# Kernel optimization log

Hardware: AMD Instinct MI355X
Metric: run time of the kernel (lower is better)

Reference implementation:

```python
import jax, jax.numpy as jnp
import numpy as np

NDIM = 3        # coordinate dimensionality
KS = 3          # kernel size per dim (odd)
DIL = 0.05      # dilation (spacing between kernel cells)
MAXD = 1.0      # max_distance cap on SDF values
G = 64          # SDF grid resolution per dim
NSDF = 8        # number of SDF grids
OUT = 32        # out_channels
K = KS ** NDIM  # 27 kernel cells
CELL = 0.031    # grid cell size -> grid extent ~2.0


def _kernel_offsets():
    r = (jnp.arange(KS, dtype=jnp.float32) - KS // 2) * DIL
    ox, oy, oz = jnp.meshgrid(r, r, r, indexing='ij')
    return jnp.stack([ox.ravel(), oy.ravel(), oz.ravel()], -1)  # [K,3]


def _rot_inv(q, v):
    # rotate v by the inverse of quaternion q (xyzw layout), broadcasting
    u = -q[..., :3]
    w = q[..., 3:4]
    c = jnp.cross(u, v)
    return v + 2.0 * jnp.cross(u, c + w * v)


def setup_inputs() -> dict:
    key = jax.random.key(0)
    ks = jax.random.split(key, 8)
    B, N, M = 2, 50000, 4
    extent = G * CELL  # ~2.0, local grid extent
    locs = jax.random.uniform(ks[0], (B, N, NDIM), jnp.float32) * extent
    idxs = jax.random.randint(ks[1], (B, M), 0, NSDF).astype(jnp.int32)
    trans = jax.random.uniform(ks[2], (B, M, NDIM), jnp.float32) * 0.2
    quat = jax.random.normal(ks[3], (B, M, 4), jnp.float32)
    quat = quat / jnp.linalg.norm(quat, axis=-1, keepdims=True)
    poses = jnp.concatenate([trans, quat], axis=-1)  # [B,M,7] = trans + quat(xyzw)
    scales = jax.random.uniform(ks[4], (B, M), jnp.float32) + 0.5
    sdf_grid = jax.random.normal(ks[5], (NSDF, G, G, G), jnp.float32) * 0.3 + 0.2
    cell_sizes = jnp.full((NSDF,), CELL, jnp.float32)
    weight = jax.random.normal(ks[6], (OUT, K), jnp.float32) * 0.1
    bias = jax.random.normal(ks[7], (OUT,), jnp.float32) * 0.1
    return dict(locs=locs, idxs=idxs, poses=poses, scales=scales,
                sdf_grid=sdf_grid, cell_sizes=cell_sizes, weight=weight, bias=bias)


def _convsdf(locs, idxs, poses, scales, sdf_grid, cell_sizes, weight, bias):
    offs = _kernel_offsets()                                  # [K,3]
    p = locs[:, :, None, :] + offs[None, None, :, :]          # [B,N,K,3] kernel-cell points
    t = poses[:, :, :NDIM]                                    # [B,M,3]
    q = poses[:, :, NDIM:]                                    # [B,M,4]
    # transform each kernel-cell point into each SDF's local frame
    r = p[:, :, :, None, :] - t[:, None, None, :, :]          # [B,N,K,M,3]
    r = _rot_inv(q[:, None, None, :, :], r)
    sc = scales[:, None, None, :, None]                       # [B,1,1,M,1]
    r = r / sc
    cs = cell_sizes[idxs][:, None, None, :, None]             # [B,1,1,M,1]
    gc = r / cs - 0.5                                         # grid coords (values at cell centers)
    inb = jnp.all((r >= 0.0) & (r <= G * cs), axis=-1)        # [B,N,K,M] inside grid?
    gcc = jnp.clip(gc, 0.0, G - 1.0)
    i0 = jnp.clip(jnp.floor(gcc), 0.0, G - 2.0).astype(jnp.int32)
    fr = gcc - i0.astype(jnp.float32)
    flat = sdf_grid.reshape(-1)
    jb = idxs.astype(jnp.int32)[:, None, None, :]             # [B,1,1,M]
    val = jnp.zeros(inb.shape, jnp.float32)
    # trilinear interpolation: 8 corner gathers
    for dx in (0, 1):
        wx = fr[..., 0] if dx else 1.0 - fr[..., 0]
        for dy in (0, 1):
            wy = fr[..., 1] if dy else 1.0 - fr[..., 1]
            for dz in (0, 1):
                wz = fr[..., 2] if dz else 1.0 - fr[..., 2]
                fi = ((jb * G + i0[..., 0] + dx) * G + i0[..., 1] + dy) * G + i0[..., 2] + dz
                val = val + wx * wy * wz * jnp.take(flat, fi)
    # scaled SDF value; out-of-grid -> max_distance, then min over objects, cap
    val = jnp.where(inb, val * sc[..., 0], MAXD)
    d = jnp.minimum(jnp.min(val, axis=-1), MAXD)              # [B,N,K]
    return jnp.einsum('bnk,ok->bno', d, weight) + bias        # [B,N,OUT]


def reference(locs, idxs, poses, scales, sdf_grid, cell_sizes, weight, bias):
    return _convsdf(locs, idxs, poses, scales, sdf_grid, cell_sizes, weight, bias)
```

## Files before the change

### kernel.cpp

```cpp
#include <hip/hip_runtime.h>
#include <math.h>

#define KK 27
#define MM 4
#define OUTC 32
#define GG 64
#define DILF 0.05f
#define MAXDF 1.0f
#define MU 4e-3f

static __device__ inline bool exact_inb(float lx, float ly, float lz,
                                        float ox, float oy, float oz,
                                        float tx, float ty, float tz,
                                        float qx, float qy, float qz, float qw,
                                        float sc, float gcs) {
#pragma clang fp contract(off)
    float px = lx + ox, py = ly + oy, pz = lz + oz;
    float vx = px - tx, vy = py - ty, vz = pz - tz;
    float ux = -qx, uy = -qy, uz = -qz;
    float cx = uy * vz - uz * vy;
    float cy = uz * vx - ux * vz;
    float cz = ux * vy - uy * vx;
    float twx = cx + qw * vx;
    float twy = cy + qw * vy;
    float twz = cz + qw * vz;
    float rx = vx + 2.0f * (uy * twz - uz * twy);
    float ry = vy + 2.0f * (uz * twx - ux * twz);
    float rz = vz + 2.0f * (ux * twy - uy * twx);
    rx = rx / sc; ry = ry / sc; rz = rz / sc;
    return (rx >= 0.0f) & (rx <= gcs) & (ry >= 0.0f) & (ry <= gcs) &
           (rz >= 0.0f) & (rz <= gcs);
}

__global__ __launch_bounds__(256) void convsdf_kernel(
    const float* __restrict__ locs, const int* __restrict__ idxs,
    const float* __restrict__ poses, const float* __restrict__ scales,
    const float* __restrict__ sdf, const float* __restrict__ cells,
    const float* __restrict__ weight, const float* __restrict__ bias,
    float* __restrict__ out, int N) {
    __shared__ float4 s_ro[MM][KK];
    __shared__ float4 s_off[KK];
    __shared__ float4 s_wT4[KK * OUTC / 4];
    __shared__ float  s_bias[OUTC];
    __shared__ float  s_t[MM][3];
    __shared__ float  s_q[MM][4];
    __shared__ float  s_sc[MM];
    __shared__ float  s_gcs[MM];
    __shared__ float  s_invscs[MM];
    __shared__ int    s_goff[MM];

    const int b = blockIdx.y;
    const int tid = threadIdx.x;

    float* s_wT = (float*)s_wT4;
    for (int i = tid; i < KK * OUTC; i += 256) {
        int k = i >> 5, o = i & 31;
        s_wT[i] = weight[o * KK + k];
    }
    if (tid < OUTC) s_bias[tid] = bias[tid];
    if (tid < KK) {
        int kx = tid / 9, ky = (tid / 3) % 3, kz = tid % 3;
        s_off[tid] = make_float4((float)(kx - 1) * DILF, (float)(ky - 1) * DILF,
                                 (float)(kz - 1) * DILF, 0.0f);
    }
    if (tid >= 128 && tid < 128 + MM) {
        int m = tid - 128;
        const float* pp = poses + (b * MM + m) * 7;
        float sc = scales[b * MM + m];
        int gi = idxs[b * MM + m];
        float cs = cells[gi];
        s_t[m][0] = pp[0]; s_t[m][1] = pp[1]; s_t[m][2] = pp[2];
        s_q[m][0] = pp[3]; s_q[m][1] = pp[4]; s_q[m][2] = pp[5]; s_q[m][3] = pp[6];
        s_sc[m] = sc;
        s_gcs[m] = (float)GG * cs;
        s_invscs[m] = 1.0f / (sc * cs);
        s_goff[m] = gi * GG * GG * GG;
    }
    __syncthreads();

    if (tid < MM * KK) {
        int m = tid / KK, k = tid - m * KK;
        float4 off = s_off[k];
        float qx = s_q[m][0], qy = s_q[m][1], qz = s_q[m][2], qw = s_q[m][3];
        float ux = -qx, uy = -qy, uz = -qz;
        float vx = off.x, vy = off.y, vz = off.z;
        float cx = uy * vz - uz * vy + qw * vx;
        float cy = uz * vx - ux * vz + qw * vy;
        float cz = ux * vy - uy * vx + qw * vz;
        float rx = vx + 2.0f * (uy * cz - uz * cy);
        float ry = vy + 2.0f * (uz * cx - ux * cz);
        float rz = vz + 2.0f * (ux * cy - uy * cx);
        float f = s_invscs[m];
        s_ro[m][k] = make_float4(rx * f, ry * f, rz * f, 0.0f);
    }
    __syncthreads();

    const int pl = tid >> 2;
    const int m  = tid & 3;
    const int n  = blockIdx.x * 64 + pl;
    if (n >= N) return;

    const float* lp = locs + (size_t)(b * N + n) * 3;
    float lx = lp[0], ly = lp[1], lz = lp[2];

    float tx = s_t[m][0], ty = s_t[m][1], tz = s_t[m][2];
    float qx = s_q[m][0], qy = s_q[m][1], qz = s_q[m][2], qw = s_q[m][3];
    float sc = s_sc[m], gcs = s_gcs[m];
    float bux, buy, buz;
    {
        float vx = lx - tx, vy = ly - ty, vz = lz - tz;
        float ux = -qx, uy = -qy, uz = -qz;
        float cx = uy * vz - uz * vy + qw * vx;
        float cy = uz * vx - ux * vz + qw * vy;
        float cz = ux * vy - uy * vx + qw * vz;
        float rx = vx + 2.0f * (uy * cz - uz * cy);
        float ry = vy + 2.0f * (uz * cx - ux * cz);
        float rz = vz + 2.0f * (ux * cy - uy * cx);
        float f = s_invscs[m];
        bux = rx * f; buy = ry * f; buz = rz * f;
    }
    const float* gbase = sdf + s_goff[m];

    float acc[8];
#pragma unroll
    for (int j = 0; j < 8; ++j) acc[j] = s_bias[m * 8 + j];

#pragma unroll 3
    for (int k = 0; k < KK; ++k) {
        float4 ro = s_ro[m][k];
        float ux = bux + ro.x;
        float uy = buy + ro.y;
        float uz = buz + ro.z;
        float mn = fminf(fminf(ux, uy), uz);
        float mx = fmaxf(fmaxf(ux, uy), uz);
        bool inb = (mn >= 0.0f) & (mx <= 64.0f);
        float a0 = fminf(fminf(fabsf(ux), fabsf(uy)), fabsf(uz));
        float a1 = fminf(fminf(fabsf(ux - 64.0f), fabsf(uy - 64.0f)),
                         fabsf(uz - 64.0f));
        if (fminf(a0, a1) < MU) {
            float4 ofk = s_off[k];
            inb = exact_inb(lx, ly, lz, ofk.x, ofk.y, ofk.z,
                            tx, ty, tz, qx, qy, qz, qw, sc, gcs);
        }
        float v = MAXDF;
        if (inb) {
            float gx = fminf(fmaxf(ux - 0.5f, 0.0f), 63.0f);
            float gy = fminf(fmaxf(uy - 0.5f, 0.0f), 63.0f);
            float gz = fminf(fmaxf(uz - 0.5f, 0.0f), 63.0f);
            int ix = min((int)gx, 62);
            int iy = min((int)gy, 62);
            int iz = min((int)gz, 62);
            float fx = gx - (float)ix;
            float fy = gy - (float)iy;
            float fz = gz - (float)iz;
            const float* g = gbase + ((ix * GG + iy) * GG + iz);
            float v000 = g[0], v001 = g[1];
            float v010 = g[GG], v011 = g[GG + 1];
            float v100 = g[GG * GG], v101 = g[GG * GG + 1];
            float v110 = g[GG * GG + GG], v111 = g[GG * GG + GG + 1];
            float c00 = v000 + fz * (v001 - v000);
            float c01 = v010 + fz * (v011 - v010);
            float c10 = v100 + fz * (v101 - v100);
            float c11 = v110 + fz * (v111 - v110);
            float c0 = c00 + fy * (c01 - c00);
            float c1 = c10 + fy * (c11 - c10);
            v = (c0 + fx * (c1 - c0)) * sc;
        }
        float dk = v;
        dk = fminf(dk, __shfl_xor(dk, 1, 4));
        dk = fminf(dk, __shfl_xor(dk, 2, 4));
        float4 w0 = s_wT4[k * (OUTC / 4) + m * 2 + 0];
        float4 w1 = s_wT4[k * (OUTC / 4) + m * 2 + 1];
        acc[0] += dk * w0.x; acc[1] += dk * w0.y;
        acc[2] += dk * w0.z; acc[3] += dk * w0.w;
        acc[4] += dk * w1.x; acc[5] += dk * w1.y;
        acc[6] += dk * w1.z; acc[7] += dk * w1.w;
    }

    float* op = out + (size_t)(b * N + n) * OUTC + m * 8;
    *(float4*)&op[0] = make_float4(acc[0], acc[1], acc[2], acc[3]);
    *(float4*)&op[4] = make_float4(acc[4], acc[5], acc[6], acc[7]);
}

extern "C" void kernel_launch(void* const* d_in, const int* in_sizes, int n_in,
                              void* d_out, int out_size, void* d_ws, size_t ws_size,
                              hipStream_t stream) {
    const float* locs   = (const float*)d_in[0];
    const int*   idxs   = (const int*)d_in[1];
    const float* poses  = (const float*)d_in[2];
    const float* scales = (const float*)d_in[3];
    const float* sdf    = (const float*)d_in[4];
    const float* cells  = (const float*)d_in[5];
    const float* weight = (const float*)d_in[6];
    const float* bias   = (const float*)d_in[7];
    float* out = (float*)d_out;

    int B = in_sizes[1] / MM;
    int N = in_sizes[0] / (3 * B);

    dim3 grid((N + 63) / 64, B);
    convsdf_kernel<<<grid, 256, 0, stream>>>(locs, idxs, poses, scales, sdf,
                                             cells, weight, bias, out, N);
}
```

Measured before the change: 28.68 us.

## Repack SDF grids into fp16 corner-octet layout for single-load trilinear gathers

Adds a per-call repack kernel that stores all eight trilinear corner values of each voxel as packed fp16 in one 16-byte record, restricted to grids referenced by idxs. The main kernel then fetches one uint4 per sample instead of eight scattered floats. This is meant to cut gather latency and transaction count, at the cost of an extra kernel launch, tens of MB of workspace writes each call, and fp16 rounding of SDF values. It falls back to the direct kernel when the workspace is too small.

Result: slower. 35.58 us (+24.1%).

```diff
diff --git a/kernel.cpp b/kernel.cpp
--- a/kernel.cpp
+++ b/kernel.cpp
@@ -1,10 +1,12 @@
 #include <hip/hip_runtime.h>
+#include <hip/hip_fp16.h>
 #include <math.h>
 
 #define KK 27
 #define MM 4
 #define OUTC 32
 #define GG 64
+#define GG3 (GG * GG * GG)
 #define DILF 0.05f
 #define MAXDF 1.0f
 #define MU 4e-3f
@@ -32,7 +34,194 @@
            (rz >= 0.0f) & (rz <= gcs);
 }
 
-__global__ __launch_bounds__(256) void convsdf_kernel(
+__global__ __launch_bounds__(256) void repack_kernel(
+    const float* __restrict__ sdf, const int* __restrict__ idxs,
+    uint4* __restrict__ oct, int nslots) {
+    const int j = blockIdx.y;
+    __shared__ int ref;
+    if (threadIdx.x == 0) {
+        int r = 0;
+        for (int s = 0; s < nslots; ++s) r |= (idxs[s] == j) ? 1 : 0;
+        ref = r;
+    }
+    __syncthreads();
+    if (!ref) return;
+
+    int i = blockIdx.x * 256 + threadIdx.x;
+    int x = i >> 12, y = (i >> 6) & 63, z = i & 63;
+    int xp = min(x + 1, 63), yp = min(y + 1, 63), zp = min(z + 1, 63);
+    const float* g = sdf + (size_t)j * GG3;
+    float v000 = g[(x * GG + y) * GG + z];
+    float v001 = g[(x * GG + y) * GG + zp];
+    float v010 = g[(x * GG + yp) * GG + z];
+    float v011 = g[(x * GG + yp) * GG + zp];
+    float v100 = g[(xp * GG + y) * GG + z];
+    float v101 = g[(xp * GG + y) * GG + zp];
+    float v110 = g[(xp * GG + yp) * GG + z];
+    float v111 = g[(xp * GG + yp) * GG + zp];
+    __half2 h0 = __floats2half2_rn(v000, v001);
+    __half2 h1 = __floats2half2_rn(v010, v011);
+    __half2 h2 = __floats2half2_rn(v100, v101);
+    __half2 h3 = __floats2half2_rn(v110, v111);
+    uint4 o;
+    o.x = *(unsigned int*)&h0;
+    o.y = *(unsigned int*)&h1;
+    o.z = *(unsigned int*)&h2;
+    o.w = *(unsigned int*)&h3;
+    oct[(size_t)j * GG3 + i] = o;
+}
+
+__global__ __launch_bounds__(256) void convsdf_oct_kernel(
+    const float* __restrict__ locs, const int* __restrict__ idxs,
+    const float* __restrict__ poses, const float* __restrict__ scales,
+    const uint4* __restrict__ oct, const float* __restrict__ cells,
+    const float* __restrict__ weight, const float* __restrict__ bias,
+    float* __restrict__ out, int N) {
+    __shared__ float4 s_ro[MM][KK];
+    __shared__ float4 s_off[KK];
+    __shared__ float4 s_wT4[KK * OUTC / 4];
+    __shared__ float  s_bias[OUTC];
+    __shared__ float  s_t[MM][3];
+    __shared__ float  s_q[MM][4];
+    __shared__ float  s_sc[MM];
+    __shared__ float  s_gcs[MM];
+    __shared__ float  s_invscs[MM];
+    __shared__ int    s_goff[MM];
+
+    const int b = blockIdx.y;
+    const int tid = threadIdx.x;
+
+    float* s_wT = (float*)s_wT4;
+    for (int i = tid; i < KK * OUTC; i += 256) {
+        int k = i >> 5, o = i & 31;
+        s_wT[i] = weight[o * KK + k];
+    }
+    if (tid < OUTC) s_bias[tid] = bias[tid];
+    if (tid < KK) {
+        int kx = tid / 9, ky = (tid / 3) % 3, kz = tid % 3;
+        s_off[tid] = make_float4((float)(kx - 1) * DILF, (float)(ky - 1) * DILF,
+                                 (float)(kz - 1) * DILF, 0.0f);
+    }
+    if (tid >= 128 && tid < 128 + MM) {
+        int m = tid - 128;
+        const float* pp = poses + (b * MM + m) * 7;
+        float sc = scales[b * MM + m];
+        int gi = idxs[b * MM + m];
+        float cs = cells[gi];
+        s_t[m][0] = pp[0]; s_t[m][1] = pp[1]; s_t[m][2] = pp[2];
+        s_q[m][0] = pp[3]; s_q[m][1] = pp[4]; s_q[m][2] = pp[5]; s_q[m][3] = pp[6];
+        s_sc[m] = sc;
+        s_gcs[m] = (float)GG * cs;
+        s_invscs[m] = 1.0f / (sc * cs);
+        s_goff[m] = gi * GG3;
+    }
+    __syncthreads();
+
+    if (tid < MM * KK) {
+        int m = tid / KK, k = tid - m * KK;
+        float4 off = s_off[k];
+        float qx = s_q[m][0], qy = s_q[m][1], qz = s_q[m][2], qw = s_q[m][3];
+        float ux = -qx, uy = -qy, uz = -qz;
+        float vx = off.x, vy = off.y, vz = off.z;
+        float cx = uy * vz - uz * vy + qw * vx;
+        float cy = uz * vx - ux * vz + qw * vy;
+        float cz = ux * vy - uy * vx + qw * vz;
+        float rx = vx + 2.0f * (uy * cz - uz * cy);
+        float ry = vy + 2.0f * (uz * cx - ux * cz);
+        float rz = vz + 2.0f * (ux * cy - uy * cx);
+        float f = s_invscs[m];
+        s_ro[m][k] = make_float4(rx * f, ry * f, rz * f, 0.0f);
+    }
+    __syncthreads();
+
+    const int pl = tid >> 2;
+    const int m  = tid & 3;
+    const int n  = blockIdx.x * 64 + pl;
+    if (n >= N) return;
+
+    const float* lp = locs + (size_t)(b * N + n) * 3;
+    float lx = lp[0], ly = lp[1], lz = lp[2];
+
+    float tx = s_t[m][0], ty = s_t[m][1], tz = s_t[m][2];
+    float qx = s_q[m][0], qy = s_q[m][1], qz = s_q[m][2], qw = s_q[m][3];
+    float sc = s_sc[m], gcs = s_gcs[m];
+    float bux, buy, buz;
+    {
+        float vx = lx - tx, vy = ly - ty, vz = lz - tz;
+        float ux = -qx, uy = -qy, uz = -qz;
+        float cx = uy * vz - uz * vy + qw * vx;
+        float cy = uz * vx - ux * vz + qw * vy;
+        float cz = ux * vy - uy * vx + qw * vz;
+        float rx = vx + 2.0f * (uy * cz - uz * cy);
+        float ry = vy + 2.0f * (uz * cx - ux * cz);
+        float rz = vz + 2.0f * (ux * cy - uy * cx);
+        float f = s_invscs[m];
+        bux = rx * f; buy = ry * f; buz = rz * f;
+    }
+    const uint4* octg = oct + s_goff[m];
+
+    float acc[8];
+#pragma unroll
+    for (int j = 0; j < 8; ++j) acc[j] = s_bias[m * 8 + j];
+
+#pragma unroll 3
+    for (int k = 0; k < KK; ++k) {
+        float4 ro = s_ro[m][k];
+        float ux = bux + ro.x;
+        float uy = buy + ro.y;
+        float uz = buz + ro.z;
+        float mn = fminf(fminf(ux, uy), uz);
+        float mx = fmaxf(fmaxf(ux, uy), uz);
+        bool inb = (mn >= 0.0f) & (mx <= 64.0f);
+        float a0 = fminf(fminf(fabsf(ux), fabsf(uy)), fabsf(uz));
+        float a1 = fminf(fminf(fabsf(ux - 64.0f), fabsf(uy - 64.0f)),
+                         fabsf(uz - 64.0f));
+        if (fminf(a0, a1) < MU) {
+            float4 ofk = s_off[k];
+            inb = exact_inb(lx, ly, lz, ofk.x, ofk.y, ofk.z,
+                            tx, ty, tz, qx, qy, qz, qw, sc, gcs);
+        }
+        float v = MAXDF;
+        if (inb) {
+            float gx = fminf(fmaxf(ux - 0.5f, 0.0f), 63.0f);
+            float gy = fminf(fmaxf(uy - 0.5f, 0.0f), 63.0f);
+            float gz = fminf(fmaxf(uz - 0.5f, 0.0f), 63.0f);
+            int ix = min((int)gx, 62);
+            int iy = min((int)gy, 62);
+            int iz = min((int)gz, 62);
+            float fx = gx - (float)ix;
+            float fy = gy - (float)iy;
+            float fz = gz - (float)iz;
+            uint4 o = octg[(ix * GG + iy) * GG + iz];
+            float2 p00 = __half22float2(*(__half2*)&o.x);
+            float2 p01 = __half22float2(*(__half2*)&o.y);
+            float2 p10 = __half22float2(*(__half2*)&o.z);
+            float2 p11 = __half22float2(*(__half2*)&o.w);
+            float c00 = p00.x + fz * (p00.y - p00.x);
+            float c01 = p01.x + fz * (p01.y - p01.x);
+            float c10 = p10.x + fz * (p10.y - p10.x);
+            float c11 = p11.x + fz * (p11.y - p11.x);
+            float c0 = c00 + fy * (c01 - c00);
+            float c1 = c10 + fy * (c11 - c10);
+            v = (c0 + fx * (c1 - c0)) * sc;
+        }
+        float dk = v;
+        dk = fminf(dk, __shfl_xor(dk, 1, 4));
+        dk = fminf(dk, __shfl_xor(dk, 2, 4));
+        float4 w0 = s_wT4[k * (OUTC / 4) + m * 2 + 0];
+        float4 w1 = s_wT4[k * (OUTC / 4) + m * 2 + 1];
+        acc[0] += dk * w0.x; acc[1] += dk * w0.y;
+        acc[2] += dk * w0.z; acc[3] += dk * w0.w;
+        acc[4] += dk * w1.x; acc[5] += dk * w1.y;
+        acc[6] += dk * w1.z; acc[7] += dk * w1.w;
+    }
+
+    float* op = out + (size_t)(b * N + n) * OUTC + m * 8;
+    *(float4*)&op[0] = make_float4(acc[0], acc[1], acc[2], acc[3]);
+    *(float4*)&op[4] = make_float4(acc[4], acc[5], acc[6], acc[7]);
+}
+
+__global__ __launch_bounds__(256) void convsdf_direct_kernel(
     const float* __restrict__ locs, const int* __restrict__ idxs,
     const float* __restrict__ poses, const float* __restrict__ scales,
     const float* __restrict__ sdf, const float* __restrict__ cells,
@@ -74,7 +263,7 @@
         s_sc[m] = sc;
         s_gcs[m] = (float)GG * cs;
         s_invscs[m] = 1.0f / (sc * cs);
-        s_goff[m] = gi * GG * GG * GG;
+        s_goff[m] = gi * GG3;
     }
     __syncthreads();
 
@@ -197,8 +386,22 @@
 
     int B = in_sizes[1] / MM;
     int N = in_sizes[0] / (3 * B);
-
+    int NSDF = in_sizes[4] / GG3;
+    int nslots = in_sizes[1];
+
+    size_t oct_bytes = (size_t)NSDF * GG3 * 16;
     dim3 grid((N + 63) / 64, B);
-    convsdf_kernel<<<grid, 256, 0, stream>>>(locs, idxs, poses, scales, sdf,
-                                             cells, weight, bias, out, N);
+
+    if (ws_size >= oct_bytes) {
+        uint4* oct = (uint4*)d_ws;
+        dim3 gridR(GG3 / 256, NSDF);
+        repack_kernel<<<gridR, 256, 0, stream>>>(sdf, idxs, oct, nslots);
+        convsdf_oct_kernel<<<grid, 256, 0, stream>>>(locs, idxs, poses, scales,
+                                                     oct, cells, weight, bias,
+                                                     out, N);
+    } else {
+        convsdf_direct_kernel<<<grid, 256, 0, stream>>>(locs, idxs, poses,
+                                                        scales, sdf, cells,
+                                                        weight, bias, out, N);
+    }
 }
```

## Spatially bin points via counting sort to improve SDF gather locality

Applied to the files above, without the earlier changes.

Adds four pre-kernels (zero, histogram, single-block scan, scatter) that counting-sort the points into a 16^3 spatial bin order per batch. The main kernel then processes points in that order, so neighbouring threads gather nearby SDF voxels and cache reuse should improve. The cost is four extra launches, atomics, a serial single-block scan, and scattered output writes. The bin scale hardcodes the test's cell size of 0.031.

New measurement: 50.10 us. +74.6%, slower.

```diff
diff --git a/kernel.cpp b/kernel.cpp
--- a/kernel.cpp
+++ b/kernel.cpp
@@ -5,9 +5,12 @@
 #define MM 4
 #define OUTC 32
 #define GG 64
+#define GG3 (GG * GG * GG)
 #define DILF 0.05f
 #define MAXDF 1.0f
 #define MU 4e-3f
+#define NBIN1 16
+#define NBINS (NBIN1 * NBIN1 * NBIN1)
 
 static __device__ inline bool exact_inb(float lx, float ly, float lz,
                                         float ox, float oy, float oz,
@@ -32,12 +35,74 @@
            (rz >= 0.0f) & (rz <= gcs);
 }
 
+static __device__ inline int point_bin(const float* __restrict__ locs,
+                                       int b, int n, int N, float sbin) {
+    const float* lp = locs + (size_t)(b * N + n) * 3;
+    int bx = (int)(lp[0] * sbin); bx = bx < 0 ? 0 : (bx > 15 ? 15 : bx);
+    int by = (int)(lp[1] * sbin); by = by < 0 ? 0 : (by > 15 ? 15 : by);
+    int bz = (int)(lp[2] * sbin); bz = bz < 0 ? 0 : (bz > 15 ? 15 : bz);
+    return b * NBINS + ((bx << 8) | (by << 4) | bz);
+}
+
+__global__ __launch_bounds__(256) void zero_kernel(int* __restrict__ hist, int n) {
+    int i = blockIdx.x * 256 + threadIdx.x;
+    if (i < n) hist[i] = 0;
+}
+
+__global__ __launch_bounds__(256) void hist_kernel(
+    const float* __restrict__ locs, int* __restrict__ hist,
+    int N, int total, float sbin) {
+    int i = blockIdx.x * 256 + threadIdx.x;
+    if (i >= total) return;
+    int b = i / N, n = i - b * N;
+    atomicAdd(&hist[point_bin(locs, b, n, N, sbin)], 1);
+}
+
+__global__ __launch_bounds__(1024) void scan_kernel(int* __restrict__ hist,
+                                                    int nbins) {
+    __shared__ int part[1024];
+    int t = threadIdx.x;
+    int chunk = (nbins + 1023) / 1024;
+    int base = t * chunk;
+    int v[16];
+    int s = 0;
+    for (int j = 0; j < chunk; ++j) {
+        int idx = base + j;
+        v[j] = (idx < nbins) ? hist[idx] : 0;
+        s += v[j];
+    }
+    part[t] = s;
+    __syncthreads();
+    for (int off = 1; off < 1024; off <<= 1) {
+        int x = (t >= off) ? part[t - off] : 0;
+        __syncthreads();
+        part[t] += x;
+        __syncthreads();
+    }
+    int ex = part[t] - s;
+    for (int j = 0; j < chunk; ++j) {
+        int idx = base + j;
+        if (idx < nbins) hist[idx] = ex;
+        ex += v[j];
+    }
+}
+
+__global__ __launch_bounds__(256) void scatter_kernel(
+    const float* __restrict__ locs, int* __restrict__ cursor,
+    int* __restrict__ perm, int N, int total, float sbin) {
+    int i = blockIdx.x * 256 + threadIdx.x;
+    if (i >= total) return;
+    int b = i / N, n = i - b * N;
+    int pos = atomicAdd(&cursor[point_bin(locs, b, n, N, sbin)], 1);
+    perm[pos] = n;
+}
+
 __global__ __launch_bounds__(256) void convsdf_kernel(
     const float* __restrict__ locs, const int* __restrict__ idxs,
     const float* __restrict__ poses, const float* __restrict__ scales,
     const float* __restrict__ sdf, const float* __restrict__ cells,
     const float* __restrict__ weight, const float* __restrict__ bias,
-    float* __restrict__ out, int N) {
+    const int* __restrict__ perm, float* __restrict__ out, int N) {
     __shared__ float4 s_ro[MM][KK];
     __shared__ float4 s_off[KK];
     __shared__ float4 s_wT4[KK * OUTC / 4];
@@ -74,7 +139,7 @@
         s_sc[m] = sc;
         s_gcs[m] = (float)GG * cs;
         s_invscs[m] = 1.0f / (sc * cs);
-        s_goff[m] = gi * GG * GG * GG;
+        s_goff[m] = gi * GG3;
     }
     __syncthreads();
 
@@ -97,8 +162,9 @@
 
     const int pl = tid >> 2;
     const int m  = tid & 3;
-    const int n  = blockIdx.x * 64 + pl;
-    if (n >= N) return;
+    const int s_idx = blockIdx.x * 64 + pl;
+    if (s_idx >= N) return;
+    const int n = perm[b * N + s_idx];
 
     const float* lp = locs + (size_t)(b * N + n) * 3;
     float lx = lp[0], ly = lp[1], lz = lp[2];
@@ -197,8 +263,21 @@
 
     int B = in_sizes[1] / MM;
     int N = in_sizes[0] / (3 * B);
+    int total = B * N;
+    int nbins = B * NBINS;
+
+    int* hist = (int*)d_ws;
+    int* perm = hist + nbins;
+
+    float sbin = (float)NBIN1 / ((float)GG * 0.031f);
+
+    zero_kernel<<<(nbins + 255) / 256, 256, 0, stream>>>(hist, nbins);
+    hist_kernel<<<(total + 255) / 256, 256, 0, stream>>>(locs, hist, N, total, sbin);
+    scan_kernel<<<1, 1024, 0, stream>>>(hist, nbins);
+    scatter_kernel<<<(total + 255) / 256, 256, 0, stream>>>(locs, hist, perm,
+                                                            N, total, sbin);
 
     dim3 grid((N + 63) / 64, B);
     convsdf_kernel<<<grid, 256, 0, stream>>>(locs, idxs, poses, scales, sdf,
-                                             cells, weight, bias, out, N);
-}
+                                             cells, weight, bias, perm, out, N);
+}
```
